# Optimization experiments

Hardware: AMD Instinct MI355X
Metric: run time of the kernel (lower is better)

The kernel has to match this reference:

```python
import jax, jax.numpy as jnp
import numpy as np

GROUP_SIZE = 128  # quantization group size along K


def setup_inputs() -> dict:
    key = jax.random.key(0)
    k1, k2, k3, k4 = jax.random.split(key, 4)
    B, S, K = 2, 2048, 4096
    N = 11008
    num_groups = K // GROUP_SIZE
    x = jax.random.normal(k1, (B, S, K), dtype=jnp.float32)
    # int8 quantized weights, stored as int32 for portability (values in [-128, 127])
    qw = jax.random.randint(k2, (N, K), -128, 128, dtype=jnp.int32)
    # per-group scales (positive, small, like amax/127)
    sw = jax.random.uniform(k3, (N, num_groups), dtype=jnp.float32, minval=1e-4, maxval=0.02)
    bias = jax.random.normal(k4, (N,), dtype=jnp.float32)
    return {"x": x, "qw": qw, "sw": sw, "bias": bias}


def reference(x, qw, sw, bias):
    # x: [..., K], qw: [N, K] int8-valued, sw: [N, K//GROUP_SIZE], bias: [N]
    N, K = qw.shape
    num_groups = K // GROUP_SIZE
    # per-group dequantize: w[n, g, j] = qw[n, g, j] * sw[n, g]
    w_dequant = (qw.reshape(N, num_groups, GROUP_SIZE).astype(jnp.float32)
                 * sw[:, :, None]).reshape(N, K)
    x_dtype = x.dtype
    y = jnp.einsum('...k,nk->...n', x.astype(jnp.float32), w_dequant).astype(x_dtype)
    y = y + bias
    return y
```

## Files before the change

### kernel.cpp

```cpp
#include <hip/hip_runtime.h>


typedef __attribute__((ext_vector_type(8))) short short8;
typedef __attribute__((ext_vector_type(4))) float floatx4;

__device__ __forceinline__ unsigned short f2bf_rne(float f) {
  union { float f; unsigned int u; } c;
  c.f = f;
  unsigned int u = c.u;
  u += 0x7FFFu + ((u >> 16) & 1u);
  return (unsigned short)(u >> 16);
}

__global__ void prep_kernel(const float* __restrict__ x,
                            const int* __restrict__ qw,
                            const float* __restrict__ sw,
                            short* __restrict__ xb,
                            short* __restrict__ wb,
                            long nx_chunks, long total_chunks,
                            int K, int G, int ngroups) {
  long stride = (long)gridDim.x * blockDim.x;
  for (long c = (long)blockIdx.x * blockDim.x + threadIdx.x;
       c < total_chunks; c += stride) {
    if (c < nx_chunks) {
      long i = c * 8;
      const float4* p = (const float4*)(x + i);
      float4 a = p[0], b = p[1];
      short8 o;
      o[0] = (short)f2bf_rne(a.x); o[1] = (short)f2bf_rne(a.y);
      o[2] = (short)f2bf_rne(a.z); o[3] = (short)f2bf_rne(a.w);
      o[4] = (short)f2bf_rne(b.x); o[5] = (short)f2bf_rne(b.y);
      o[6] = (short)f2bf_rne(b.z); o[7] = (short)f2bf_rne(b.w);
      *(short8*)(xb + i) = o;
    } else {
      long e = (c - nx_chunks) * 8;
      int n = (int)(e / K);
      int k = (int)(e - (long)n * K);
      const int* q = qw + (long)n * K + k;
      float s = sw[(long)n * ngroups + k / G];
      int4 q0 = *(const int4*)q;
      int4 q1 = *(const int4*)(q + 4);
      short8 o;
      o[0] = (short)f2bf_rne((float)q0.x * s);
      o[1] = (short)f2bf_rne((float)q0.y * s);
      o[2] = (short)f2bf_rne((float)q0.z * s);
      o[3] = (short)f2bf_rne((float)q0.w * s);
      o[4] = (short)f2bf_rne((float)q1.x * s);
      o[5] = (short)f2bf_rne((float)q1.y * s);
      o[6] = (short)f2bf_rne((float)q1.z * s);
      o[7] = (short)f2bf_rne((float)q1.w * s);
      *(short8*)(wb + e) = o;
    }
  }
}

#define BM 128
#define BN 128
#define BK 32


__global__ __launch_bounds__(256, 4) void gemm_bt_kernel(
    const short* __restrict__ Xb,
    const short* __restrict__ Wb,
    const float* __restrict__ bias,
    float* __restrict__ Y,
    int M, int N, int K) {
  __shared__ short As[BM * BK];
  __shared__ short Bs[BN * BK];

  const int t = threadIdx.x;
  const int wave = t >> 6;
  const int lane = t & 63;
  const int wm = wave >> 1;
  const int wn = wave & 1;
  const int quad = lane >> 4;
  const int l16 = lane & 15;

  const int gn = gridDim.x, gm = gridDim.y;
  int mt, nt;
  if ((gm & 7) == 0) {
    int stripe = gm >> 3;
    int bid = blockIdx.y * gn + blockIdx.x;
    int xcd = bid & 7;
    int q = bid >> 3;
    int msub = q % stripe;
    nt = q / stripe;
    mt = xcd * stripe + msub;
  } else {
    mt = blockIdx.y; nt = blockIdx.x;
  }
  const int tileM = mt * BM;
  const int tileN = nt * BN;

  floatx4 acc[4][4];
#pragma unroll
  for (int i = 0; i < 4; i++)
#pragma unroll
    for (int j = 0; j < 4; j++) acc[i][j] = {0.f, 0.f, 0.f, 0.f};

  const int srow = t >> 2;
  const int scol = ((t & 3) ^ ((t >> 3) & 3)) * 8;

  const short* Ag = Xb + (long)tileM * K;
  const short* Bg = Wb + (long)tileN * K;

  const int cswz = (quad ^ ((l16 >> 1) & 3)) * 8;

  for (int k0 = 0; k0 < K; k0 += BK) {
#pragma unroll
    for (int i = 0; i < 2; ++i) {
      __builtin_amdgcn_global_load_lds(
          (const __attribute__((address_space(1))) void*)(Ag + (long)(i * 64 + srow) * K + k0 + scol),
          (__attribute__((address_space(3))) void*)(As + i * 64 * BK + t * 8),
          16, 0, 0);
    }
#pragma unroll
    for (int i = 0; i < 2; ++i) {
      __builtin_amdgcn_global_load_lds(
          (const __attribute__((address_space(1))) void*)(Bg + (long)(i * 64 + srow) * K + k0 + scol),
          (__attribute__((address_space(3))) void*)(Bs + i * 64 * BK + t * 8),
          16, 0, 0);
    }
    __syncthreads();

    const short* Aw = As + wm * 64 * BK;
    const short* Bw = Bs + wn * 64 * BK;
    short8 af[4], bf[4];
#pragma unroll
    for (int i = 0; i < 4; i++)
      af[i] = *(const short8*)(Aw + (i * 16 + l16) * BK + cswz);
#pragma unroll
    for (int j = 0; j < 4; j++)
      bf[j] = *(const short8*)(Bw + (j * 16 + l16) * BK + cswz);

#pragma unroll
    for (int i = 0; i < 4; i++)
#pragma unroll
      for (int j = 0; j < 4; j++)
        acc[i][j] = __builtin_amdgcn_mfma_f32_16x16x32_bf16(af[i], bf[j],
                                                            acc[i][j], 0, 0, 0);
    __syncthreads();
  }

  const int mbase = tileM + wm * 64;
  const int nbase = tileN + wn * 64;
#pragma unroll
  for (int i = 0; i < 4; i++) {
#pragma unroll
    for (int j = 0; j < 4; j++) {
      int n = nbase + j * 16 + l16;
      float bv = bias[n];
#pragma unroll
      for (int r = 0; r < 4; r++) {
        int m = mbase + i * 16 + quad * 4 + r;
        Y[(long)m * N + n] = acc[i][j][r] + bv;
      }
    }
  }
}

__global__ void naive_kernel(const float* __restrict__ x,
                             const int* __restrict__ qw,
                             const float* __restrict__ sw,
                             const float* __restrict__ bias,
                             float* __restrict__ y,
                             int M, int N, int K, int G) {
  long idx = (long)blockIdx.x * blockDim.x + threadIdx.x;
  if (idx >= (long)M * N) return;
  int m = (int)(idx / N), n = (int)(idx % N);
  int ng = K / G;
  float acc = 0.f;
  for (int g = 0; g < ng; g++) {
    float s = sw[(long)n * ng + g];
    float part = 0.f;
    for (int k = g * G; k < (g + 1) * G; k++)
      part += x[(long)m * K + k] * (float)qw[(long)n * K + k];
    acc += part * s;
  }
  y[idx] = acc + bias[n];
}

extern "C" void kernel_launch(void* const* d_in, const int* in_sizes, int n_in,
                              void* d_out, int out_size, void* d_ws, size_t ws_size,
                              hipStream_t stream) {
  const float* x = (const float*)d_in[0];
  const int* qw = (const int*)d_in[1];
  const float* sw = (const float*)d_in[2];
  const float* bias = (const float*)d_in[3];
  float* y = (float*)d_out;

  const int N = in_sizes[3];
  const int K = in_sizes[1] / N;
  const int M = in_sizes[0] / K;
  const int ngroups = in_sizes[2] / N;
  const int G = K / ngroups;

  const long MK = (long)M * K;
  const long NK = (long)N * K;
  const size_t need = (size_t)(MK + NK) * sizeof(short);

  if (ws_size < need || (M % BM) || (N % BN) || (K % BK) || (G % 8)) {
    long total = (long)M * N;
    naive_kernel<<<(unsigned)((total + 255) / 256), 256, 0, stream>>>(
        x, qw, sw, bias, y, M, N, K, G);
    return;
  }

  short* xb = (short*)d_ws;
  short* wb = xb + MK;

  long nx_chunks = MK / 8;
  long total_chunks = nx_chunks + NK / 8;
  prep_kernel<<<2048, 256, 0, stream>>>(x, qw, sw, xb, wb,
                                        nx_chunks, total_chunks, K, G, ngroups);

  dim3 grid((unsigned)(N / BN), (unsigned)(M / BM));
  gemm_bt_kernel<<<grid, 256, 0, stream>>>(xb, wb, bias, y, M, N, K);
}
```

Before: 735.5 us.

## Replace GEMM with 256x256 double-buffered 8-wave pipelined MFMA kernel

Replaces the 128x128x32 single-buffered GEMM with a 256x256x64 tile kernel using 512 threads (8 waves). Global-to-LDS loads go into double-buffered, XOR-swizzled shared memory and are interleaved with four MFMA phases per K-step. The schedule is fenced by explicit waitcnt, sched_barrier and setprio calls so loads overlap compute and per-tile global traffic drops. The prep kernel also swaps divisions for shifts when K and G are powers of two. In exchange, the larger LDS footprint and register use limit occupancy, and 688 blocks give a partial last wave.

```diff
diff --git a/kernel.cpp b/kernel.cpp
--- a/kernel.cpp
+++ b/kernel.cpp
@@ -18,7 +18,7 @@
                             short* __restrict__ xb,
                             short* __restrict__ wb,
                             long nx_chunks, long total_chunks,
-                            int K, int G, int ngroups) {
+                            int K, int kshift, int gshift, int G, int ngroups) {
   long stride = (long)gridDim.x * blockDim.x;
   for (long c = (long)blockIdx.x * blockDim.x + threadIdx.x;
        c < total_chunks; c += stride) {
@@ -34,10 +34,17 @@
       *(short8*)(xb + i) = o;
     } else {
       long e = (c - nx_chunks) * 8;
-      int n = (int)(e / K);
-      int k = (int)(e - (long)n * K);
+      int n, k;
+      if (kshift >= 0) {
+        n = (int)(e >> kshift);
+        k = (int)(e & (long)(K - 1));
+      } else {
+        n = (int)(e / K);
+        k = (int)(e - (long)n * K);
+      }
+      int g = (gshift >= 0) ? (k >> gshift) : (k / G);
       const int* q = qw + (long)n * K + k;
-      float s = sw[(long)n * ngroups + k / G];
+      float s = sw[(long)n * ngroups + g];
       int4 q0 = *(const int4*)q;
       int4 q1 = *(const int4*)(q + 4);
       short8 o;
@@ -54,107 +61,187 @@
   }
 }
 
-#define BM 128
-#define BN 128
-#define BK 32
-
-
-__global__ __launch_bounds__(256, 4) void gemm_bt_kernel(
+#define BM 256
+#define BN 256
+#define BK 64
+
+__device__ __forceinline__ void stage_half(const short* __restrict__ src,
+                                           int rowbase, int k0, int K,
+                                           short* dst, int t) {
+#pragma unroll
+  for (int j = 0; j < 2; ++j) {
+    const int c = (j << 9) | t;
+    const int r = c >> 3;
+    const int g = (c & 7) ^ (r & 7);
+    __builtin_amdgcn_global_load_lds(
+        (const __attribute__((address_space(1))) void*)(
+            src + (long)(rowbase + r) * K + k0 + (g << 3)),
+        (__attribute__((address_space(3))) void*)(dst + (c << 3)),
+        16, 0, 0);
+  }
+}
+
+__global__ __launch_bounds__(512, 2) void gemm8p_kernel(
     const short* __restrict__ Xb,
     const short* __restrict__ Wb,
     const float* __restrict__ bias,
     float* __restrict__ Y,
     int M, int N, int K) {
-  __shared__ short As[BM * BK];
-  __shared__ short Bs[BN * BK];
+  __shared__ short As[2][2][128 * 64];
+  __shared__ short Bs[2][2][128 * 64];
 
   const int t = threadIdx.x;
   const int wave = t >> 6;
   const int lane = t & 63;
-  const int wm = wave >> 1;
-  const int wn = wave & 1;
+  const int wm = wave >> 2;
+  const int wn = wave & 3;
   const int quad = lane >> 4;
   const int l16 = lane & 15;
 
-  const int gn = gridDim.x, gm = gridDim.y;
+  const int gm = M / BM, gn = N / BN;
+  int bid = (int)blockIdx.x;
   int mt, nt;
   if ((gm & 7) == 0) {
     int stripe = gm >> 3;
-    int bid = blockIdx.y * gn + blockIdx.x;
     int xcd = bid & 7;
     int q = bid >> 3;
-    int msub = q % stripe;
+    mt = xcd * stripe + q % stripe;
     nt = q / stripe;
-    mt = xcd * stripe + msub;
   } else {
-    mt = blockIdx.y; nt = blockIdx.x;
-  }
-  const int tileM = mt * BM;
-  const int tileN = nt * BN;
-
-  floatx4 acc[4][4];
-#pragma unroll
-  for (int i = 0; i < 4; i++)
-#pragma unroll
-    for (int j = 0; j < 4; j++) acc[i][j] = {0.f, 0.f, 0.f, 0.f};
-
-  const int srow = t >> 2;
-  const int scol = ((t & 3) ^ ((t >> 3) & 3)) * 8;
-
-  const short* Ag = Xb + (long)tileM * K;
-  const short* Bg = Wb + (long)tileN * K;
-
-  const int cswz = (quad ^ ((l16 >> 1) & 3)) * 8;
-
-  for (int k0 = 0; k0 < K; k0 += BK) {
-#pragma unroll
-    for (int i = 0; i < 2; ++i) {
-      __builtin_amdgcn_global_load_lds(
-          (const __attribute__((address_space(1))) void*)(Ag + (long)(i * 64 + srow) * K + k0 + scol),
-          (__attribute__((address_space(3))) void*)(As + i * 64 * BK + t * 8),
-          16, 0, 0);
-    }
-#pragma unroll
-    for (int i = 0; i < 2; ++i) {
-      __builtin_amdgcn_global_load_lds(
-          (const __attribute__((address_space(1))) void*)(Bg + (long)(i * 64 + srow) * K + k0 + scol),
-          (__attribute__((address_space(3))) void*)(Bs + i * 64 * BK + t * 8),
-          16, 0, 0);
-    }
-    __syncthreads();
-
-    const short* Aw = As + wm * 64 * BK;
-    const short* Bw = Bs + wn * 64 * BK;
-    short8 af[4], bf[4];
-#pragma unroll
-    for (int i = 0; i < 4; i++)
-      af[i] = *(const short8*)(Aw + (i * 16 + l16) * BK + cswz);
-#pragma unroll
-    for (int j = 0; j < 4; j++)
-      bf[j] = *(const short8*)(Bw + (j * 16 + l16) * BK + cswz);
-
-#pragma unroll
-    for (int i = 0; i < 4; i++)
-#pragma unroll
-      for (int j = 0; j < 4; j++)
-        acc[i][j] = __builtin_amdgcn_mfma_f32_16x16x32_bf16(af[i], bf[j],
+    mt = bid % gm;
+    nt = bid / gm;
+  }
+  const long tileM = (long)mt * BM;
+  const long tileN = (long)nt * BN;
+
+  const short* __restrict__ Ag = Xb + tileM * K;
+  const short* __restrict__ Bg = Wb + tileN * K;
+
+  floatx4 acc[8][4];
+#pragma unroll
+  for (int i = 0; i < 8; ++i)
+#pragma unroll
+    for (int j = 0; j < 4; ++j) acc[i][j] = {0.f, 0.f, 0.f, 0.f};
+
+  const int NT = K / BK;
+
+  stage_half(Ag,   0,  0, K, &As[0][0][0], t);
+  stage_half(Ag, 128,  0, K, &As[0][1][0], t);
+  stage_half(Bg,   0,  0, K, &Bs[0][0][0], t);
+  stage_half(Bg, 128,  0, K, &Bs[0][1][0], t);
+  stage_half(Ag,   0, BK, K, &As[1][0][0], t);
+  stage_half(Ag, 128, BK, K, &As[1][1][0], t);
+  asm volatile("s_waitcnt vmcnt(4)" ::: "memory");
+  __builtin_amdgcn_sched_barrier(0);
+  __builtin_amdgcn_s_barrier();
+
+  const int c0 = (quad ^ (l16 & 7)) << 3;
+  const int c1 = c0 ^ 32;
+  const int nb = (wn & 1) * 64;
+
+  for (int T = 0; T < NT; ++T) {
+    const int buf = T & 1;
+    const short* Ab = &As[buf][wm][0];
+    const short* Bb = &Bs[buf][wn >> 1][0];
+    short8 a0[8], a1[8], b0[4], b1[4];
+
+#pragma unroll
+    for (int i = 0; i < 8; ++i)
+      a0[i] = *(const short8*)(Ab + (i * 16 + l16) * 64 + c0);
+#pragma unroll
+    for (int j = 0; j < 4; ++j)
+      b0[j] = *(const short8*)(Bb + (nb + j * 16 + l16) * 64 + c0);
+    if (T + 1 < NT)
+      stage_half(Bg, 0, (T + 1) * BK, K, &Bs[buf ^ 1][0][0], t);
+    __builtin_amdgcn_sched_barrier(0);
+    __builtin_amdgcn_s_barrier();
+    asm volatile("s_waitcnt lgkmcnt(0)" ::: "memory");
+    __builtin_amdgcn_sched_barrier(0);
+    __builtin_amdgcn_s_setprio(1);
+#pragma unroll
+    for (int i = 0; i < 4; ++i)
+#pragma unroll
+      for (int j = 0; j < 4; ++j)
+        acc[i][j] = __builtin_amdgcn_mfma_f32_16x16x32_bf16(a0[i], b0[j],
                                                             acc[i][j], 0, 0, 0);
-    __syncthreads();
-  }
-
-  const int mbase = tileM + wm * 64;
-  const int nbase = tileN + wn * 64;
-#pragma unroll
-  for (int i = 0; i < 4; i++) {
-#pragma unroll
-    for (int j = 0; j < 4; j++) {
-      int n = nbase + j * 16 + l16;
-      float bv = bias[n];
-#pragma unroll
-      for (int r = 0; r < 4; r++) {
-        int m = mbase + i * 16 + quad * 4 + r;
-        Y[(long)m * N + n] = acc[i][j][r] + bv;
-      }
+    __builtin_amdgcn_s_setprio(0);
+    __builtin_amdgcn_sched_barrier(0);
+    __builtin_amdgcn_s_barrier();
+
+#pragma unroll
+    for (int i = 0; i < 8; ++i)
+      a1[i] = *(const short8*)(Ab + (i * 16 + l16) * 64 + c1);
+#pragma unroll
+    for (int j = 0; j < 4; ++j)
+      b1[j] = *(const short8*)(Bb + (nb + j * 16 + l16) * 64 + c1);
+    if (T + 1 < NT)
+      stage_half(Bg, 128, (T + 1) * BK, K, &Bs[buf ^ 1][1][0], t);
+    __builtin_amdgcn_sched_barrier(0);
+    __builtin_amdgcn_s_barrier();
+    asm volatile("s_waitcnt lgkmcnt(0)" ::: "memory");
+    __builtin_amdgcn_sched_barrier(0);
+    __builtin_amdgcn_s_setprio(1);
+#pragma unroll
+    for (int i = 0; i < 4; ++i)
+#pragma unroll
+      for (int j = 0; j < 4; ++j)
+        acc[4 + i][j] = __builtin_amdgcn_mfma_f32_16x16x32_bf16(
+            a0[4 + i], b0[j], acc[4 + i][j], 0, 0, 0);
+    __builtin_amdgcn_s_setprio(0);
+    __builtin_amdgcn_sched_barrier(0);
+    __builtin_amdgcn_s_barrier();
+
+    if (T + 2 < NT)
+      stage_half(Ag, 0, (T + 2) * BK, K, &As[buf][0][0], t);
+    __builtin_amdgcn_sched_barrier(0);
+    __builtin_amdgcn_s_barrier();
+    asm volatile("s_waitcnt lgkmcnt(0)" ::: "memory");
+    __builtin_amdgcn_sched_barrier(0);
+    __builtin_amdgcn_s_setprio(1);
+#pragma unroll
+    for (int i = 0; i < 4; ++i)
+#pragma unroll
+      for (int j = 0; j < 4; ++j)
+        acc[i][j] = __builtin_amdgcn_mfma_f32_16x16x32_bf16(a1[i], b1[j],
+                                                            acc[i][j], 0, 0, 0);
+    __builtin_amdgcn_s_setprio(0);
+    __builtin_amdgcn_sched_barrier(0);
+    __builtin_amdgcn_s_barrier();
+
+    if (T + 2 < NT)
+      stage_half(Ag, 128, (T + 2) * BK, K, &As[buf][1][0], t);
+    __builtin_amdgcn_sched_barrier(0);
+    __builtin_amdgcn_s_barrier();
+    asm volatile("s_waitcnt lgkmcnt(0)" ::: "memory");
+    __builtin_amdgcn_sched_barrier(0);
+    __builtin_amdgcn_s_setprio(1);
+#pragma unroll
+    for (int i = 0; i < 4; ++i)
+#pragma unroll
+      for (int j = 0; j < 4; ++j)
+        acc[4 + i][j] = __builtin_amdgcn_mfma_f32_16x16x32_bf16(
+            a1[4 + i], b1[j], acc[4 + i][j], 0, 0, 0);
+    __builtin_amdgcn_s_setprio(0);
+    if (T + 2 < NT)
+      asm volatile("s_waitcnt vmcnt(4)" ::: "memory");
+    else
+      asm volatile("s_waitcnt vmcnt(0)" ::: "memory");
+    __builtin_amdgcn_sched_barrier(0);
+    __builtin_amdgcn_s_barrier();
+  }
+
+  const long mbase = tileM + wm * 128;
+  const long nbase = tileN + wn * 64;
+#pragma unroll
+  for (int j = 0; j < 4; ++j) {
+    const long n = nbase + j * 16 + l16;
+    const float bv = bias[n];
+#pragma unroll
+    for (int i = 0; i < 8; ++i) {
+      const long m0 = mbase + i * 16 + quad * 4;
+#pragma unroll
+      for (int r = 0; r < 4; ++r)
+        Y[(m0 + r) * (long)N + n] = acc[i][j][r] + bv;
     }
   }
 }
@@ -199,7 +286,8 @@
   const long NK = (long)N * K;
   const size_t need = (size_t)(MK + NK) * sizeof(short);
 
-  if (ws_size < need || (M % BM) || (N % BN) || (K % BK) || (G % 8)) {
+  if (ws_size < need || (M % BM) || (N % BN) || (K % BK) || (K < 2 * BK) ||
+      (G % 8)) {
     long total = (long)M * N;
     naive_kernel<<<(unsigned)((total + 255) / 256), 256, 0, stream>>>(
         x, qw, sw, bias, y, M, N, K, G);
@@ -211,9 +299,12 @@
 
   long nx_chunks = MK / 8;
   long total_chunks = nx_chunks + NK / 8;
+  int kshift = ((K & (K - 1)) == 0) ? __builtin_ctz((unsigned)K) : -1;
+  int gshift = ((G & (G - 1)) == 0) ? __builtin_ctz((unsigned)G) : -1;
   prep_kernel<<<2048, 256, 0, stream>>>(x, qw, sw, xb, wb,
-                                        nx_chunks, total_chunks, K, G, ngroups);
-
-  dim3 grid((unsigned)(N / BN), (unsigned)(M / BM));
-  gemm_bt_kernel<<<grid, 256, 0, stream>>>(xb, wb, bias, y, M, N, K);
-}
+                                        nx_chunks, total_chunks,
+                                        K, kshift, gshift, G, ngroups);
+
+  dim3 grid((unsigned)((M / BM) * (N / BN)));
+  gemm8p_kernel<<<grid, 512, 0, stream>>>(xb, wb, bias, y, M, N, K);
+}
```

Result: no change. 736.2 us (+0.1%).

## Double-buffer LDS tiles in GEMM and split prep into shift-indexed kernels

Applied to the files above, without the earlier changes.

The GEMM main loop now uses two LDS buffers, so the async global-to-LDS loads for the next K tile are issued before the MFMAs on the current tile. This overlaps memory latency with compute and removes one barrier per iteration. The combined prep kernel is split into separate x and weight conversion kernels, and the weight kernel uses shift/mask indexing instead of 64-bit division when K/8 and G/8 are powers of two. In exchange, the GEMM uses twice the LDS per block, which can limit how many blocks fit on each CU.

```diff
diff --git a/kernel.cpp b/kernel.cpp
--- a/kernel.cpp
+++ b/kernel.cpp
@@ -12,45 +12,53 @@
   return (unsigned short)(u >> 16);
 }
 
-__global__ void prep_kernel(const float* __restrict__ x,
-                            const int* __restrict__ qw,
-                            const float* __restrict__ sw,
-                            short* __restrict__ xb,
-                            short* __restrict__ wb,
-                            long nx_chunks, long total_chunks,
-                            int K, int G, int ngroups) {
+__global__ void prep_x_kernel(const float* __restrict__ x,
+                              short* __restrict__ xb, long nchunks) {
   long stride = (long)gridDim.x * blockDim.x;
   for (long c = (long)blockIdx.x * blockDim.x + threadIdx.x;
-       c < total_chunks; c += stride) {
-    if (c < nx_chunks) {
-      long i = c * 8;
-      const float4* p = (const float4*)(x + i);
-      float4 a = p[0], b = p[1];
-      short8 o;
-      o[0] = (short)f2bf_rne(a.x); o[1] = (short)f2bf_rne(a.y);
-      o[2] = (short)f2bf_rne(a.z); o[3] = (short)f2bf_rne(a.w);
-      o[4] = (short)f2bf_rne(b.x); o[5] = (short)f2bf_rne(b.y);
-      o[6] = (short)f2bf_rne(b.z); o[7] = (short)f2bf_rne(b.w);
-      *(short8*)(xb + i) = o;
+       c < nchunks; c += stride) {
+    const float4* p = (const float4*)(x + c * 8);
+    float4 a = p[0], b = p[1];
+    short8 o;
+    o[0] = (short)f2bf_rne(a.x); o[1] = (short)f2bf_rne(a.y);
+    o[2] = (short)f2bf_rne(a.z); o[3] = (short)f2bf_rne(a.w);
+    o[4] = (short)f2bf_rne(b.x); o[5] = (short)f2bf_rne(b.y);
+    o[6] = (short)f2bf_rne(b.z); o[7] = (short)f2bf_rne(b.w);
+    *(short8*)(xb + c * 8) = o;
+  }
+}
+
+__global__ void prep_w_kernel(const int* __restrict__ qw,
+                              const float* __restrict__ sw,
+                              short* __restrict__ wb, long nchunks,
+                              int kc, int kcshift, int gc, int gcshift,
+                              int ngroups) {
+  long stride = (long)gridDim.x * blockDim.x;
+  for (long c = (long)blockIdx.x * blockDim.x + threadIdx.x;
+       c < nchunks; c += stride) {
+    int n, kch;
+    if (kcshift >= 0) {
+      n = (int)(c >> kcshift);
+      kch = (int)(c & (long)(kc - 1));
     } else {
-      long e = (c - nx_chunks) * 8;
-      int n = (int)(e / K);
-      int k = (int)(e - (long)n * K);
-      const int* q = qw + (long)n * K + k;
-      float s = sw[(long)n * ngroups + k / G];
-      int4 q0 = *(const int4*)q;
-      int4 q1 = *(const int4*)(q + 4);
-      short8 o;
-      o[0] = (short)f2bf_rne((float)q0.x * s);
-      o[1] = (short)f2bf_rne((float)q0.y * s);
-      o[2] = (short)f2bf_rne((float)q0.z * s);
-      o[3] = (short)f2bf_rne((float)q0.w * s);
-      o[4] = (short)f2bf_rne((float)q1.x * s);
-      o[5] = (short)f2bf_rne((float)q1.y * s);
-      o[6] = (short)f2bf_rne((float)q1.z * s);
-      o[7] = (short)f2bf_rne((float)q1.w * s);
-      *(short8*)(wb + e) = o;
+      n = (int)(c / kc);
+      kch = (int)(c - (long)n * kc);
     }
+    int g = (gcshift >= 0) ? (kch >> gcshift) : (kch / gc);
+    float s = sw[(long)n * ngroups + g];
+    const int* q = qw + c * 8;
+    int4 q0 = *(const int4*)q;
+    int4 q1 = *(const int4*)(q + 4);
+    short8 o;
+    o[0] = (short)f2bf_rne((float)q0.x * s);
+    o[1] = (short)f2bf_rne((float)q0.y * s);
+    o[2] = (short)f2bf_rne((float)q0.z * s);
+    o[3] = (short)f2bf_rne((float)q0.w * s);
+    o[4] = (short)f2bf_rne((float)q1.x * s);
+    o[5] = (short)f2bf_rne((float)q1.y * s);
+    o[6] = (short)f2bf_rne((float)q1.z * s);
+    o[7] = (short)f2bf_rne((float)q1.w * s);
+    *(short8*)(wb + c * 8) = o;
   }
 }
 
@@ -58,6 +66,27 @@
 #define BN 128
 #define BK 32
 
+
+__device__ __forceinline__ void stage_tile(const short* __restrict__ Ag,
+                                           const short* __restrict__ Bg,
+                                           int k0, int K,
+                                           short* Adst, short* Bdst,
+                                           int t, int srow, int scol) {
+#pragma unroll
+  for (int i = 0; i < 2; ++i)
+    __builtin_amdgcn_global_load_lds(
+        (const __attribute__((address_space(1))) void*)(
+            Ag + (long)(i * 64 + srow) * K + k0 + scol),
+        (__attribute__((address_space(3))) void*)(Adst + i * 64 * BK + t * 8),
+        16, 0, 0);
+#pragma unroll
+  for (int i = 0; i < 2; ++i)
+    __builtin_amdgcn_global_load_lds(
+        (const __attribute__((address_space(1))) void*)(
+            Bg + (long)(i * 64 + srow) * K + k0 + scol),
+        (__attribute__((address_space(3))) void*)(Bdst + i * 64 * BK + t * 8),
+        16, 0, 0);
+}
 
 __global__ __launch_bounds__(256, 4) void gemm_bt_kernel(
     const short* __restrict__ Xb,
@@ -65,8 +94,8 @@
     const float* __restrict__ bias,
     float* __restrict__ Y,
     int M, int N, int K) {
-  __shared__ short As[BM * BK];
-  __shared__ short Bs[BN * BK];
+  __shared__ short As[2][BM * BK];
+  __shared__ short Bs[2][BN * BK];
 
   const int t = threadIdx.x;
   const int wave = t >> 6;
@@ -106,25 +135,17 @@
 
   const int cswz = (quad ^ ((l16 >> 1) & 3)) * 8;
 
-  for (int k0 = 0; k0 < K; k0 += BK) {
-#pragma unroll
-    for (int i = 0; i < 2; ++i) {
-      __builtin_amdgcn_global_load_lds(
-          (const __attribute__((address_space(1))) void*)(Ag + (long)(i * 64 + srow) * K + k0 + scol),
-          (__attribute__((address_space(3))) void*)(As + i * 64 * BK + t * 8),
-          16, 0, 0);
-    }
-#pragma unroll
-    for (int i = 0; i < 2; ++i) {
-      __builtin_amdgcn_global_load_lds(
-          (const __attribute__((address_space(1))) void*)(Bg + (long)(i * 64 + srow) * K + k0 + scol),
-          (__attribute__((address_space(3))) void*)(Bs + i * 64 * BK + t * 8),
-          16, 0, 0);
-    }
-    __syncthreads();
-
-    const short* Aw = As + wm * 64 * BK;
-    const short* Bw = Bs + wn * 64 * BK;
+  stage_tile(Ag, Bg, 0, K, &As[0][0], &Bs[0][0], t, srow, scol);
+  __syncthreads();
+
+  int cur = 0;
+  for (int k0 = 0; k0 < K; k0 += BK, cur ^= 1) {
+    if (k0 + BK < K)
+      stage_tile(Ag, Bg, k0 + BK, K, &As[cur ^ 1][0], &Bs[cur ^ 1][0],
+                 t, srow, scol);
+
+    const short* Aw = &As[cur][0] + wm * 64 * BK;
+    const short* Bw = &Bs[cur][0] + wn * 64 * BK;
     short8 af[4], bf[4];
 #pragma unroll
     for (int i = 0; i < 4; i++)
@@ -209,10 +230,14 @@
   short* xb = (short*)d_ws;
   short* wb = xb + MK;
 
-  long nx_chunks = MK / 8;
-  long total_chunks = nx_chunks + NK / 8;
-  prep_kernel<<<2048, 256, 0, stream>>>(x, qw, sw, xb, wb,
-                                        nx_chunks, total_chunks, K, G, ngroups);
+  const int kc = K / 8;
+  const int gc = G / 8;
+  int kcshift = ((kc & (kc - 1)) == 0) ? __builtin_ctz((unsigned)kc) : -1;
+  int gcshift = ((gc & (gc - 1)) == 0) ? __builtin_ctz((unsigned)gc) : -1;
+
+  prep_x_kernel<<<2048, 256, 0, stream>>>(x, xb, MK / 8);
+  prep_w_kernel<<<2048, 256, 0, stream>>>(qw, sw, wb, NK / 8,
+                                          kc, kcshift, gc, gcshift, ngroups);
 
   dim3 grid((unsigned)(N / BN), (unsigned)(M / BM));
   gemm_bt_kernel<<<grid, 256, 0, stream>>>(xb, wb, bias, y, M, N, K);
```

Measured after the change: 741.2 us. No clear change (+0.8%).
